# Optimization experiments

Measured on AMD Instinct MI355X. Metric: run time of the kernel, lower is better.

The kernel has to match this reference:

```python
import jax, jax.numpy as jnp
import numpy as np

T, B, L = 40, 64, 80
D_IN = 256
H = 4 * D_IN  # 1024
A = 18


def _lstm_scan(x, h0, c0, W_ih, W_hh, b_ih, b_hh):
    # x: [S,B,in] -> outputs [S,B,H]; PyTorch gate order i,f,g,o
    b = b_ih + b_hh
    def step(carry, xt):
        h, c = carry
        g = xt @ W_ih.T + h @ W_hh.T + b
        i, f, gg, o = jnp.split(g, 4, axis=-1)
        c = jax.nn.sigmoid(f) * c + jax.nn.sigmoid(i) * jnp.tanh(gg)
        h = jax.nn.sigmoid(o) * jnp.tanh(c)
        return (h, c), h
    (h, c), ys = jax.lax.scan(step, (h0, c0), x)
    return ys, h, c


def setup_inputs() -> dict:
    key = jax.random.key(0)
    ks = jax.random.split(key, 24)
    def rn(k, shape, scale=0.02):
        return jax.random.normal(k, shape, dtype=jnp.float32) * scale
    return {
        "state": rn(ks[0], (T, B, D_IN), 1.0),
        "demonstration": rn(ks[1], (T, B, L, D_IN), 1.0),
        "demonstration_length": jax.random.randint(ks[2], (T, B), 1, L + 1, dtype=jnp.int32),
        "h0": jnp.zeros((B, H), jnp.float32),
        "c0": jnp.zeros((B, H), jnp.float32),
        "enc_Wih": rn(ks[3], (4 * H, D_IN)),
        "enc_Whh": rn(ks[4], (4 * H, H)),
        "enc_bih": rn(ks[5], (4 * H,)),
        "enc_bhh": rn(ks[6], (4 * H,)),
        "attn_W": rn(ks[7], (1, 2 * H)),
        "attn_b": rn(ks[8], (1,)),
        "comb_W": rn(ks[9], (H, H + D_IN)),
        "comb_b": rn(ks[10], (H,)),
        "lstm_Wih": rn(ks[11], (4 * H, H)),
        "lstm_Whh": rn(ks[12], (4 * H, H)),
        "lstm_bih": rn(ks[13], (4 * H,)),
        "lstm_bhh": rn(ks[14], (4 * H,)),
        "mid_W": rn(ks[15], (H, H)),
        "mid_b": rn(ks[16], (H,)),
        "out_W": rn(ks[17], (A, H)),
        "out_b": rn(ks[18], (A,)),
    }


def reference(state, demonstration, demonstration_length, h0, c0,
              enc_Wih, enc_Whh, enc_bih, enc_bhh,
              attn_W, attn_b, comb_W, comb_b,
              lstm_Wih, lstm_Whh, lstm_bih, lstm_bhh,
              mid_W, mid_b, out_W, out_b):
    lengths = demonstration_length[0]              # [B], only t=0 lengths used (as in original)
    demo0 = demonstration[0]                       # [B,L,D_IN], only t=0 demo used
    z = jnp.zeros((B, H), demo0.dtype)
    enc, _, _ = _lstm_scan(demo0.transpose(1, 0, 2), z, z,
                           enc_Wih, enc_Whh, enc_bih, enc_bhh)  # [L,B,H]
    enc = enc.transpose(1, 0, 2)                   # [B,L,H]
    mask = jnp.arange(L)[None, :] < lengths[:, None]  # [B,L]
    # attn(cat(enc, h)) == enc @ Wd^T + h @ Wh^T + b (split of the concat linear)
    Wd, Wh = attn_W[:, :H], attn_W[:, H:]          # [1,H] each
    score_d = (enc @ Wd.T)[..., 0] + attn_b[0]     # [B,L], constant over t
    lstm_b = lstm_bih + lstm_bhh

    def step(carry, obs_t):
        h, c = carry
        scores = score_d + h @ Wh.T                # [B,L] ([B,1] broadcast)
        scores = jnp.where(mask, scores, -jnp.inf)
        w = jax.nn.softmax(scores, axis=-1)        # masked softmax over demo steps
        attn_applied = jnp.einsum('bl,blh->bh', w, enc)
        x = jax.nn.relu(jnp.concatenate([attn_applied, obs_t], axis=-1) @ comb_W.T + comb_b)
        g = x @ lstm_Wih.T + h @ lstm_Whh.T + lstm_b
        i, f, gg, o = jnp.split(g, 4, axis=-1)
        c = jax.nn.sigmoid(f) * c + jax.nn.sigmoid(i) * jnp.tanh(gg)
        h = jax.nn.sigmoid(o) * jnp.tanh(c)
        m = h @ mid_W.T + mid_b                    # no activation between middle and output (as in source)
        q_t = m @ out_W.T + out_b
        return (h, c), q_t

    (h, c), q = jax.lax.scan(step, (h0, c0), state)  # q: [T,B,A]
    return q, h, c
```

## Files before the change

### kernel.cpp

```cpp
#include <hip/hip_runtime.h>
#include <hip/hip_bf16.h>

#define TT 40
#define BB 64
#define LL 80
#define DD 256
#define HH 1024
#define G4H 4096
#define AA 18
#define KENC 1280
#define KLSTM 2048
#define KCOMB 1280
#define QSZ (TT*BB*AA)

typedef __bf16 bf16x8 __attribute__((ext_vector_type(8)));
typedef float  f32x4  __attribute__((ext_vector_type(4)));

#define OFF_WENC   ((size_t)0)
#define OFF_WLSTM  (OFF_WENC  + (size_t)G4H*KENC*2)
#define OFF_WCOMB  (OFF_WLSTM + (size_t)G4H*KLSTM*2)
#define OFF_WMID   (OFF_WCOMB + (size_t)HH*KCOMB*2)
#define OFF_BIASE  (OFF_WMID  + (size_t)HH*HH*2)
#define OFF_BIASL  (OFF_BIASE + (size_t)G4H*4)
#define OFF_DEMO   (OFF_BIASL + (size_t)G4H*4)
#define OFF_STATE  (OFF_DEMO  + (size_t)BB*LL*DD*2)
#define OFF_ENC    (OFF_STATE + (size_t)TT*BB*DD*2)
#define OFF_HDEC   (OFF_ENC   + (size_t)BB*LL*HH*2)
#define OFF_XALL   (OFF_HDEC  + (size_t)TT*BB*HH*2)
#define OFF_MF     (OFF_XALL  + (size_t)TT*BB*HH*2)
#define OFF_ATTNS  (OFF_MF    + (size_t)TT*BB*HH*2)
#define OFF_CF     (OFF_ATTNS + (size_t)BB*HH*2)
#define OFF_HBUF   (OFF_CF    + (size_t)BB*HH*4)

__device__ __forceinline__ float sigm(float x){ return 1.f/(1.f+__expf(-x)); }

__device__ __forceinline__ float wred_sum(float v){
#pragma unroll
  for (int s=32; s>0; s>>=1) v += __shfl_xor(v, s, 64);
  return v;
}
__device__ __forceinline__ float wred_max(float v){
#pragma unroll
  for (int s=32; s>0; s>>=1) v = fmaxf(v, __shfl_xor(v, s, 64));
  return v;
}
__device__ __forceinline__ unsigned pack_bf16(float a, float b){
  unsigned short ua = __builtin_bit_cast(unsigned short, (__bf16)a);
  unsigned short ub = __builtin_bit_cast(unsigned short, (__bf16)b);
  return (unsigned)ua | ((unsigned)ub << 16);
}

#define PB1 4096
#define PB2 8192
#define PB3 13312
#define PB4 17408
#define PB5 22528
#define PB6 25088
#define PB7 25344
#define PGRID 25472
__global__ __launch_bounds__(256)
void k_prep(const float* __restrict__ enc_wih, const float* __restrict__ enc_whh,
            const float* __restrict__ enc_bih, const float* __restrict__ enc_bhh,
            const float* __restrict__ lstm_wih, const float* __restrict__ lstm_whh,
            const float* __restrict__ lstm_bih, const float* __restrict__ lstm_bhh,
            const float* __restrict__ comb_w, const float* __restrict__ mid_w,
            const float* __restrict__ demo, const float* __restrict__ state,
            char* __restrict__ ws){
  int blk = blockIdx.x, tid = threadIdx.x;
  if (blk < PB1) {
    int p = blk;
    int gate = p & 3, jj = (p >> 2) & 3, bq = p >> 4;
    int orig = gate*HH + bq*4 + jj;
    if (tid == 0) ((float*)(ws + OFF_BIASE))[p] = enc_bih[orig] + enc_bhh[orig];
    const float* s0 = enc_wih + (size_t)orig*DD;
    const float* s1 = enc_whh + (size_t)orig*HH;
    __bf16* d = (__bf16*)(ws + OFF_WENC) + (size_t)p*KENC;
    for (int k = tid; k < KENC; k += 256)
      d[k] = (__bf16)(k < DD ? s0[k] : s1[k-DD]);
  } else if (blk < PB2) {
    int p = blk - PB1;
    int gate = p & 3, jj = (p >> 2) & 3, bq = p >> 4;
    int orig = gate*HH + bq*4 + jj;
    if (tid == 0) ((float*)(ws + OFF_BIASL))[p] = lstm_bih[orig] + lstm_bhh[orig];
    const float* s0 = lstm_wih + (size_t)orig*HH;
    const float* s1 = lstm_whh + (size_t)orig*HH;
    __bf16* d = (__bf16*)(ws + OFF_WLSTM) + (size_t)p*KLSTM;
    for (int k = tid; k < KLSTM; k += 256)
      d[k] = (__bf16)(k < HH ? s0[k] : s1[k-HH]);
  } else if (blk < PB3) {
    int i = (blk - PB2)*256 + tid;
    ((__bf16*)(ws + OFF_WCOMB))[i] = (__bf16)comb_w[i];
  } else if (blk < PB4) {
    int i = (blk - PB3)*256 + tid;
    ((__bf16*)(ws + OFF_WMID))[i] = (__bf16)mid_w[i];
  } else if (blk < PB5) {
    int i = (blk - PB4)*256 + tid;
    ((__bf16*)(ws + OFF_DEMO))[i] = (__bf16)demo[i];
  } else if (blk < PB6) {
    int i = (blk - PB5)*256 + tid;
    ((__bf16*)(ws + OFF_STATE))[i] = (__bf16)state[i];
  } else if (blk < PB7) {
    int i = (blk - PB6)*256 + tid;
    ((float*)(ws + OFF_CF))[i] = 0.f;
  } else {
    int i = (blk - PB7)*256 + tid;
    ((unsigned*)(ws + OFF_HBUF))[i] = 0u;
  }
}

__global__ __launch_bounds__(1024)
void k_enc_step(const __bf16* __restrict__ demoC, const __bf16* __restrict__ wEnc,
                const float* __restrict__ bE, const __bf16* __restrict__ hR,
                __bf16* __restrict__ hW, __bf16* __restrict__ encB,
                float* __restrict__ cf, int t){
  const int bk = blockIdx.x, tid = threadIdx.x;
  const int wv = tid >> 6, ln = tid & 63;
  const int l15 = ln & 15, lhi = ln >> 4;
  const int klane = lhi * 8;
  const int mt = wv & 3, kq = wv >> 2;
  const int am = mt*16 + l15;

  __shared__ float g_lds[4][BB*17];

  const __bf16* brow = wEnc + (size_t)(bk*16 + l15)*KENC;
  const __bf16* arow = demoC + ((size_t)am*LL + t)*DD;
  const __bf16* hrow = hR + (size_t)am*HH;

  f32x4 acc = {0.f,0.f,0.f,0.f};
  const int kb = kq*320;
#pragma unroll
  for (int kk = 0; kk < 320; kk += 32) {
    int k0 = kb + kk + klane;
    const __bf16* pa = (k0 < DD) ? (arow + k0) : (hrow + (k0 - DD));
    acc = __builtin_amdgcn_mfma_f32_16x16x32_bf16(*(const bf16x8*)pa,
                                                  *(const bf16x8*)(brow + k0), acc, 0,0,0);
  }
  {
    int r0 = mt*16 + lhi*4;
#pragma unroll
    for (int r = 0; r < 4; ++r) g_lds[kq][(r0+r)*17 + l15] = acc[r];
  }
  __syncthreads();
  if (tid < 128) {
    const int m_ = tid >> 1, q2 = tid & 1;
    const int j0_ = bk*4 + 2*q2;
    int gb = m_*17 + q2*8, cb = bk*16 + q2*8;
    float g[8];
#pragma unroll
    for (int j = 0; j < 8; ++j)
      g[j] = g_lds[0][gb+j] + g_lds[1][gb+j] + g_lds[2][gb+j] + g_lds[3][gb+j] + bE[cb+j];
    float cA = cf[m_*HH + j0_], cB = cf[m_*HH + j0_ + 1];
    float cn0 = sigm(g[1])*cA + sigm(g[0])*tanhf(g[2]);
    float cn1 = sigm(g[5])*cB + sigm(g[4])*tanhf(g[6]);
    float hn0 = sigm(g[3])*tanhf(cn0);
    float hn1 = sigm(g[7])*tanhf(cn1);
    cf[m_*HH + j0_] = cn0; cf[m_*HH + j0_ + 1] = cn1;
    unsigned hp = pack_bf16(hn0, hn1);
    *(unsigned*)(hW + (size_t)m_*HH + j0_) = hp;
    *(unsigned*)(encB + ((size_t)m_*LL + t)*HH + j0_) = hp;
  }
}

__global__ __launch_bounds__(1024)
void k_dec_step(const __bf16* __restrict__ xall, const __bf16* __restrict__ wLstm,
                const float* __restrict__ bL, const __bf16* __restrict__ hR,
                __bf16* __restrict__ hW, __bf16* __restrict__ hdec,
                float* __restrict__ cf, float* __restrict__ out, int t){
  const int bk = blockIdx.x, tid = threadIdx.x;
  const int wv = tid >> 6, ln = tid & 63;
  const int l15 = ln & 15, lhi = ln >> 4;
  const int klane = lhi * 8;
  const int mt = wv & 3, kq = wv >> 2;
  const int am = mt*16 + l15;

  __shared__ float g_lds[4][BB*17];

  const __bf16* brow = wLstm + (size_t)(bk*16 + l15)*KLSTM + kq*512;
  const __bf16* arow = (kq < 2) ? (xall + ((size_t)t*BB + am)*HH + kq*512)
                                : (hR + (size_t)am*HH + (kq-2)*512);

  f32x4 acc = {0.f,0.f,0.f,0.f};
#pragma unroll
  for (int kk = 0; kk < 512; kk += 32) {
    int k0 = kk + klane;
    acc = __builtin_amdgcn_mfma_f32_16x16x32_bf16(*(const bf16x8*)(arow + k0),
                                                  *(const bf16x8*)(brow + k0), acc, 0,0,0);
  }
  {
    int r0 = mt*16 + lhi*4;
#pragma unroll
    for (int r = 0; r < 4; ++r) g_lds[kq][(r0+r)*17 + l15] = acc[r];
  }
  __syncthreads();
  if (tid < 128) {
    const int m_ = tid >> 1, q2 = tid & 1;
    const int j0_ = bk*4 + 2*q2;
    int gb = m_*17 + q2*8, cb = bk*16 + q2*8;
    float g[8];
#pragma unroll
    for (int j = 0; j < 8; ++j)
      g[j] = g_lds[0][gb+j] + g_lds[1][gb+j] + g_lds[2][gb+j] + g_lds[3][gb+j] + bL[cb+j];
    float cA = cf[m_*HH + j0_], cB = cf[m_*HH + j0_ + 1];
    float cn0 = sigm(g[1])*cA + sigm(g[0])*tanhf(g[2]);
    float cn1 = sigm(g[5])*cB + sigm(g[4])*tanhf(g[6]);
    float hn0 = sigm(g[3])*tanhf(cn0);
    float hn1 = sigm(g[7])*tanhf(cn1);
    cf[m_*HH + j0_] = cn0; cf[m_*HH + j0_ + 1] = cn1;
    unsigned hp = pack_bf16(hn0, hn1);
    *(unsigned*)(hW + (size_t)m_*HH + j0_) = hp;
    *(unsigned*)(hdec + ((size_t)t*BB + m_)*HH + j0_) = hp;
    if (t == TT-1) {
      out[QSZ + m_*HH + j0_]     = hn0;
      out[QSZ + m_*HH + j0_ + 1] = hn1;
    }
  }
}

__global__ __launch_bounds__(256)
void k_attn(const int* __restrict__ demlen, const float* __restrict__ h0,
            const float* __restrict__ c0, const float* __restrict__ attn_w,
            const __bf16* __restrict__ encB, __bf16* __restrict__ attnS,
            __bf16* __restrict__ hD0, float* __restrict__ cf){
  const int bk = blockIdx.x, tid = threadIdx.x;
  const int wv = tid >> 6, ln = tid & 63;
  __shared__ float sc_sh[LL];
  __shared__ float w_sh[LL];
  int b = bk >> 2, qq = bk & 3;
  for (int i = 0; i < 20; ++i) {
    int l = wv*20 + i;
    const __bf16* er = encB + ((size_t)b*LL + l)*HH + ln*16;
    bf16x8 e0 = *(const bf16x8*)(er);
    bf16x8 e1 = *(const bf16x8*)(er + 8);
    float part = 0.f;
#pragma unroll
    for (int j = 0; j < 8; ++j) {
      part += (float)e0[j] * attn_w[ln*16 + j];
      part += (float)e1[j] * attn_w[ln*16 + 8 + j];
    }
    part = wred_sum(part);
    if (ln == 0) sc_sh[l] = part;
  }
  __syncthreads();
  if (wv == 0) {
    int len = demlen[b];
    float s0 = (ln < len) ? sc_sh[ln] : -1e30f;
    float s1 = (ln < 16 && 64+ln < len) ? sc_sh[64+ln] : -1e30f;
    float mx = wred_max(fmaxf(s0, s1));
    float e0 = __expf(s0 - mx);
    float e1 = (ln < 16) ? __expf(s1 - mx) : 0.f;
    float inv = 1.f / wred_sum(e0 + e1);
    w_sh[ln] = e0 * inv;
    if (ln < 16) w_sh[64+ln] = e1 * inv;
  }
  __syncthreads();
  {
    int col = qq*256 + tid;
    float a = 0.f;
    const __bf16* eb = encB + (size_t)b*LL*HH + col;
#pragma unroll 4
    for (int l = 0; l < LL; ++l) a += w_sh[l] * (float)eb[(size_t)l*HH];
    attnS[(size_t)b*HH + col] = (__bf16)a;
  }
  int gtid = bk*256 + tid;
  for (int i = gtid; i < BB*HH/2; i += 256*256) {
    int i2 = i*2;
    *((unsigned*)hD0 + i) = pack_bf16(h0[i2], h0[i2+1]);
  }
  for (int i = gtid; i < BB*HH; i += 256*256) cf[i] = c0[i];
}

__global__ __launch_bounds__(256)
void k_x(const __bf16* __restrict__ attnS, const __bf16* __restrict__ stateB,
         const __bf16* __restrict__ wComb, const float* __restrict__ comb_b,
         __bf16* __restrict__ xall){
  const int bk = blockIdx.x, tid = threadIdx.x;
  const int wv = tid >> 6, ln = tid & 63;
  const int l15 = ln & 15, lhi = ln >> 4;
  const int klane = lhi * 8;
  int g = bk*4 + wv;
  for (int i = 0; i < 10; ++i) {
    int ti = i*1024 + g;
    int mtt = ti >> 6, nt = ti & 63;
    f32x4 acc = {0.f,0.f,0.f,0.f};
    const __bf16* brow = wComb + (size_t)(nt*16 + l15)*KCOMB;
    int r = mtt*16 + l15, bb = r & 63;
    const __bf16* aat = attnS + (size_t)bb*HH;
    const __bf16* ast = stateB + (size_t)r*DD;
#pragma unroll 8
    for (int kk = 0; kk < KCOMB; kk += 32) {
      int k0 = kk + klane;
      bf16x8 af = (k0 < HH) ? *(const bf16x8*)(aat + k0)
                            : *(const bf16x8*)(ast + (k0-HH));
      acc = __builtin_amdgcn_mfma_f32_16x16x32_bf16(af, *(const bf16x8*)(brow + k0), acc, 0,0,0);
    }
    int col = nt*16 + l15;
    float cb = comb_b[col];
    int r0 = mtt*16 + lhi*4;
#pragma unroll
    for (int rr = 0; rr < 4; ++rr)
      xall[(size_t)(r0+rr)*HH + col] = (__bf16)fmaxf(acc[rr]+cb, 0.f);
  }
}

__global__ __launch_bounds__(256)
void k_mid(const __bf16* __restrict__ hdec, const __bf16* __restrict__ wMid,
           const float* __restrict__ mid_b, __bf16* __restrict__ mf){
  const int bk = blockIdx.x, tid = threadIdx.x;
  const int wv = tid >> 6, ln = tid & 63;
  const int l15 = ln & 15, lhi = ln >> 4;
  const int klane = lhi * 8;
  int g = bk*4 + wv;
  for (int i = 0; i < 10; ++i) {
    int ti = i*1024 + g;
    int mtt = ti >> 6, nt = ti & 63;
    f32x4 acc = {0.f,0.f,0.f,0.f};
    const __bf16* brow = wMid + (size_t)(nt*16 + l15)*HH;
    const __bf16* arow = hdec + (size_t)(mtt*16 + l15)*HH;
#pragma unroll 8
    for (int kk = 0; kk < HH; kk += 32) {
      int k0 = kk + klane;
      acc = __builtin_amdgcn_mfma_f32_16x16x32_bf16(*(const bf16x8*)(arow + k0),
                                                    *(const bf16x8*)(brow + k0), acc, 0,0,0);
    }
    int col = nt*16 + l15;
    float mb = mid_b[col];
    int r0 = mtt*16 + lhi*4;
#pragma unroll
    for (int rr = 0; rr < 4; ++rr)
      mf[(size_t)(r0+rr)*HH + col] = (__bf16)(acc[rr]+mb);
  }
}

__global__ __launch_bounds__(256)
void k_out(const __bf16* __restrict__ mf, const float* __restrict__ out_w,
           const float* __restrict__ out_b, const float* __restrict__ cf,
           float* __restrict__ out){
  const int bk = blockIdx.x, tid = threadIdx.x;
  const int wv = tid >> 6, ln = tid & 63;
  int g = bk*4 + wv;
  for (int i = 0; i < 3; ++i) {
    int row = i*1024 + g;
    if (row < TT*BB) {
      const __bf16* mr = mf + (size_t)row*HH;
      float mreg[16];
#pragma unroll
      for (int k = 0; k < 16; ++k) mreg[k] = (float)mr[ln + 64*k];
      for (int a = 0; a < AA; ++a) {
        float p = 0.f;
#pragma unroll
        for (int k = 0; k < 16; ++k) p += mreg[k] * out_w[(size_t)a*HH + ln + 64*k];
        p = wred_sum(p);
        if (ln == 0) out[(size_t)row*AA + a] = p + out_b[a];
      }
    }
  }
  for (int i = bk*256 + tid; i < BB*HH; i += 256*256)
    out[QSZ + BB*HH + i] = cf[i];
}

extern "C" void kernel_launch(void* const* d_in, const int* in_sizes, int n_in,
                              void* d_out, int out_size, void* d_ws, size_t ws_size,
                              hipStream_t stream) {
  (void)in_sizes; (void)n_in; (void)out_size; (void)ws_size;
  const float* state    = (const float*)d_in[0];
  const float* demo     = (const float*)d_in[1];
  const int*   demlen   = (const int*)d_in[2];
  const float* h0       = (const float*)d_in[3];
  const float* c0       = (const float*)d_in[4];
  const float* enc_wih  = (const float*)d_in[5];
  const float* enc_whh  = (const float*)d_in[6];
  const float* enc_bih  = (const float*)d_in[7];
  const float* enc_bhh  = (const float*)d_in[8];
  const float* attn_w   = (const float*)d_in[9];
  const float* comb_w   = (const float*)d_in[11];
  const float* comb_b   = (const float*)d_in[12];
  const float* lstm_wih = (const float*)d_in[13];
  const float* lstm_whh = (const float*)d_in[14];
  const float* lstm_bih = (const float*)d_in[15];
  const float* lstm_bhh = (const float*)d_in[16];
  const float* mid_w    = (const float*)d_in[17];
  const float* mid_b    = (const float*)d_in[18];
  const float* out_w    = (const float*)d_in[19];
  const float* out_b    = (const float*)d_in[20];
  char* ws = (char*)d_ws;

  __bf16* wEnc  = (__bf16*)(ws + OFF_WENC);
  __bf16* wLstm = (__bf16*)(ws + OFF_WLSTM);
  __bf16* wComb = (__bf16*)(ws + OFF_WCOMB);
  __bf16* wMid  = (__bf16*)(ws + OFF_WMID);
  float*  bE    = (float*)(ws + OFF_BIASE);
  float*  bL    = (float*)(ws + OFF_BIASL);
  __bf16* demoC = (__bf16*)(ws + OFF_DEMO);
  __bf16* stateB= (__bf16*)(ws + OFF_STATE);
  __bf16* encB  = (__bf16*)(ws + OFF_ENC);
  __bf16* hdec  = (__bf16*)(ws + OFF_HDEC);
  __bf16* xall  = (__bf16*)(ws + OFF_XALL);
  __bf16* mf    = (__bf16*)(ws + OFF_MF);
  __bf16* attnS = (__bf16*)(ws + OFF_ATTNS);
  float*  cf    = (float*)(ws + OFF_CF);
  __bf16* hbE0  = (__bf16*)(ws + OFF_HBUF);
  __bf16* hbE1  = hbE0 + (size_t)BB*HH;
  __bf16* hbD0  = hbE1 + (size_t)BB*HH;
  __bf16* hbD1  = hbD0 + (size_t)BB*HH;
  float*  out   = (float*)d_out;

  k_prep<<<PGRID, 256, 0, stream>>>(enc_wih, enc_whh, enc_bih, enc_bhh,
                                    lstm_wih, lstm_whh, lstm_bih, lstm_bhh,
                                    comb_w, mid_w, demo, state, ws);
  for (int t = 0; t < LL; ++t) {
    __bf16* hR = (t & 1) ? hbE1 : hbE0;
    __bf16* hW = (t & 1) ? hbE0 : hbE1;
    k_enc_step<<<256, 1024, 0, stream>>>(demoC, wEnc, bE, hR, hW, encB, cf, t);
  }
  k_attn<<<256, 256, 0, stream>>>(demlen, h0, c0, attn_w, encB, attnS, hbD0, cf);
  k_x<<<256, 256, 0, stream>>>(attnS, stateB, wComb, comb_b, xall);
  for (int t = 0; t < TT; ++t) {
    __bf16* hR = (t & 1) ? hbD1 : hbD0;
    __bf16* hW = (t & 1) ? hbD0 : hbD1;
    k_dec_step<<<256, 1024, 0, stream>>>(xall, wLstm, bL, hR, hW, hdec, cf, out, t);
  }
  k_mid<<<256, 256, 0, stream>>>(hdec, wMid, mid_b, mf);
  k_out<<<256, 256, 0, stream>>>(mf, out_w, out_b, cf, out);
}
```

Before: 1.910 ms.

## Replace per-step LSTM launches with persistent kernels using per-group flag barriers

The 80 encoder and 40 decoder per-timestep launches become two persistent kernels of 512 blocks. The batch is split into 8 independent groups of 8 rows, and each group syncs through flag-based barriers, so only blocks sharing batch rows wait on each other. The cell state now lives in registers, and h is written to a rotating per-timestep buffer with system-coherent stores. This removes launch overhead and global c round-trips, but wastes half of each 16-row MFMA tile, relies on all 512 blocks being co-resident, and has a spin timeout that could silently break correctness.

```diff
diff --git a/kernel.cpp b/kernel.cpp
--- a/kernel.cpp
+++ b/kernel.cpp
@@ -12,6 +12,13 @@
 #define KLSTM 2048
 #define KCOMB 1280
 #define QSZ (TT*BB*AA)
+
+#define GROUPS 8
+#define GBLK 64
+#define NBLK (GROUPS*GBLK)
+#define NSLOT_E (LL+1)
+#define NSLOT_D (TT+1)
+#define FLAG_STRIDE 16
 
 typedef __bf16 bf16x8 __attribute__((ext_vector_type(8)));
 typedef float  f32x4  __attribute__((ext_vector_type(4)));
@@ -29,8 +36,8 @@
 #define OFF_XALL   (OFF_HDEC  + (size_t)TT*BB*HH*2)
 #define OFF_MF     (OFF_XALL  + (size_t)TT*BB*HH*2)
 #define OFF_ATTNS  (OFF_MF    + (size_t)TT*BB*HH*2)
-#define OFF_CF     (OFF_ATTNS + (size_t)BB*HH*2)
-#define OFF_HBUF   (OFF_CF    + (size_t)BB*HH*4)
+#define OFF_HROT   (OFF_ATTNS + (size_t)BB*HH*2)
+#define OFF_BAR    (OFF_HROT  + (size_t)GROUPS*(NSLOT_E+NSLOT_D)*8*HH*2)
 
 __device__ __forceinline__ float sigm(float x){ return 1.f/(1.f+__expf(-x)); }
 
@@ -44,10 +51,34 @@
   for (int s=32; s>0; s>>=1) v = fmaxf(v, __shfl_xor(v, s, 64));
   return v;
 }
-__device__ __forceinline__ unsigned pack_bf16(float a, float b){
-  unsigned short ua = __builtin_bit_cast(unsigned short, (__bf16)a);
-  unsigned short ub = __builtin_bit_cast(unsigned short, (__bf16)b);
-  return (unsigned)ua | ((unsigned)ub << 16);
+
+__device__ __forceinline__ void st_b16_sc(__bf16* p, float v){
+  unsigned short u = __builtin_bit_cast(unsigned short, (__bf16)v);
+  asm volatile("global_store_short %0, %1, off sc0 sc1"
+               :: "v"(p), "v"((unsigned)u) : "memory");
+}
+
+__device__ __forceinline__ void grp_arrive(unsigned* flags, unsigned target, int bk){
+  __syncthreads();
+  if (threadIdx.x == 0) {
+    __builtin_amdgcn_fence(__ATOMIC_RELEASE, "agent");
+    __hip_atomic_store(flags + (size_t)bk*FLAG_STRIDE, target,
+                       __ATOMIC_RELAXED, __HIP_MEMORY_SCOPE_AGENT);
+  }
+}
+__device__ __forceinline__ void grp_wait(unsigned* flags, unsigned target, int g){
+  if (threadIdx.x < 64) {
+    unsigned long long spins = 0;
+    for (;;) {
+      unsigned a = __hip_atomic_load(flags + (size_t)(g*GBLK + threadIdx.x)*FLAG_STRIDE,
+                                     __ATOMIC_RELAXED, __HIP_MEMORY_SCOPE_AGENT);
+      if (__all((int)(a >= target))) break;
+      if (++spins > (1ull<<20)) break;
+      __builtin_amdgcn_s_sleep(1);
+    }
+  }
+  __syncthreads();
+  asm volatile("" ::: "memory");
 }
 
 #define PB1 4096
@@ -56,8 +87,8 @@
 #define PB4 17408
 #define PB5 22528
 #define PB6 25088
-#define PB7 25344
-#define PGRID 25472
+#define PB7 25216
+#define PGRID 25280
 __global__ __launch_bounds__(256)
 void k_prep(const float* __restrict__ enc_wih, const float* __restrict__ enc_whh,
             const float* __restrict__ enc_bih, const float* __restrict__ enc_bhh,
@@ -101,126 +132,138 @@
     ((__bf16*)(ws + OFF_STATE))[i] = (__bf16)state[i];
   } else if (blk < PB7) {
     int i = (blk - PB6)*256 + tid;
-    ((float*)(ws + OFF_CF))[i] = 0.f;
+    int g = i >> 12, r = i & 4095;
+    ((unsigned*)(ws + OFF_HROT))[(size_t)g*(NSLOT_E*8*HH/2) + r] = 0u;
   } else {
     int i = (blk - PB7)*256 + tid;
-    ((unsigned*)(ws + OFF_HBUF))[i] = 0u;
-  }
-}
-
-__global__ __launch_bounds__(1024)
-void k_enc_step(const __bf16* __restrict__ demoC, const __bf16* __restrict__ wEnc,
-                const float* __restrict__ bE, const __bf16* __restrict__ hR,
-                __bf16* __restrict__ hW, __bf16* __restrict__ encB,
-                float* __restrict__ cf, int t){
-  const int bk = blockIdx.x, tid = threadIdx.x;
+    ((unsigned*)(ws + OFF_BAR))[i] = 0u;
+  }
+}
+
+__global__ __launch_bounds__(256, 2)
+void k_enc(const __bf16* __restrict__ demoC, const __bf16* __restrict__ wEnc,
+           const float* __restrict__ bE, __bf16* __restrict__ hrotE,
+           __bf16* __restrict__ encB, unsigned* __restrict__ flagsE){
+  const int bk = blockIdx.x, tid = threadIdx.x;
+  const int g = bk >> 6, b64 = bk & 63;
   const int wv = tid >> 6, ln = tid & 63;
   const int l15 = ln & 15, lhi = ln >> 4;
   const int klane = lhi * 8;
-  const int mt = wv & 3, kq = wv >> 2;
-  const int am = mt*16 + l15;
-
-  __shared__ float g_lds[4][BB*17];
-
-  const __bf16* brow = wEnc + (size_t)(bk*16 + l15)*KENC;
-  const __bf16* arow = demoC + ((size_t)am*LL + t)*DD;
-  const __bf16* hrow = hR + (size_t)am*HH;
-
-  f32x4 acc = {0.f,0.f,0.f,0.f};
-  const int kb = kq*320;
-#pragma unroll
-  for (int kk = 0; kk < 320; kk += 32) {
-    int k0 = kb + kk + klane;
-    const __bf16* pa = (k0 < DD) ? (arow + k0) : (hrow + (k0 - DD));
-    acc = __builtin_amdgcn_mfma_f32_16x16x32_bf16(*(const bf16x8*)pa,
-                                                  *(const bf16x8*)(brow + k0), acc, 0,0,0);
-  }
-  {
-    int r0 = mt*16 + lhi*4;
-#pragma unroll
-    for (int r = 0; r < 4; ++r) g_lds[kq][(r0+r)*17 + l15] = acc[r];
-  }
-  __syncthreads();
-  if (tid < 128) {
-    const int m_ = tid >> 1, q2 = tid & 1;
-    const int j0_ = bk*4 + 2*q2;
-    int gb = m_*17 + q2*8, cb = bk*16 + q2*8;
-    float g[8];
-#pragma unroll
-    for (int j = 0; j < 8; ++j)
-      g[j] = g_lds[0][gb+j] + g_lds[1][gb+j] + g_lds[2][gb+j] + g_lds[3][gb+j] + bE[cb+j];
-    float cA = cf[m_*HH + j0_], cB = cf[m_*HH + j0_ + 1];
-    float cn0 = sigm(g[1])*cA + sigm(g[0])*tanhf(g[2]);
-    float cn1 = sigm(g[5])*cB + sigm(g[4])*tanhf(g[6]);
-    float hn0 = sigm(g[3])*tanhf(cn0);
-    float hn1 = sigm(g[7])*tanhf(cn1);
-    cf[m_*HH + j0_] = cn0; cf[m_*HH + j0_ + 1] = cn1;
-    unsigned hp = pack_bf16(hn0, hn1);
-    *(unsigned*)(hW + (size_t)m_*HH + j0_) = hp;
-    *(unsigned*)(encB + ((size_t)m_*LL + t)*HH + j0_) = hp;
-  }
-}
-
-__global__ __launch_bounds__(1024)
-void k_dec_step(const __bf16* __restrict__ xall, const __bf16* __restrict__ wLstm,
-                const float* __restrict__ bL, const __bf16* __restrict__ hR,
-                __bf16* __restrict__ hW, __bf16* __restrict__ hdec,
-                float* __restrict__ cf, float* __restrict__ out, int t){
-  const int bk = blockIdx.x, tid = threadIdx.x;
+  const int mb = l15 & 7;
+  const int batch = g*8 + mb;
+
+  __shared__ float g_lds[8][68];
+
+  const __bf16* brow = wEnc + (size_t)(b64*64 + wv*16 + l15)*KENC;
+  const __bf16* drow = demoC + (size_t)batch*LL*DD;
+  __bf16* hbase = hrotE + (size_t)g*NSLOT_E*8*HH;
+
+  const int em = tid >> 4, ec = tid & 15;
+  const int ecol = b64*16 + ec;
+  const int ebatch = g*8 + em;
+  float creg = 0.f;
+
+  for (int t = 0; t < LL; ++t) {
+    const __bf16* hR = hbase + (size_t)t*8*HH + (size_t)mb*HH;
+    const __bf16* arow = drow + (size_t)t*DD;
+    f32x4 acc = {0.f,0.f,0.f,0.f};
+#pragma unroll 8
+    for (int kk = 0; kk < KENC; kk += 32) {
+      int k0 = kk + klane;
+      const __bf16* pa = (k0 < DD) ? (arow + k0) : (hR + (k0 - DD));
+      acc = __builtin_amdgcn_mfma_f32_16x16x32_bf16(*(const bf16x8*)pa,
+                                                    *(const bf16x8*)(brow + k0), acc, 0,0,0);
+    }
+    {
+      int r0 = lhi*4;
+#pragma unroll
+      for (int r = 0; r < 4; ++r) {
+        int row = r0 + r;
+        if (row < 8) g_lds[row][wv*16 + l15] = acc[r];
+      }
+    }
+    __syncthreads();
+    if (tid < 128) {
+      int pb = b64*64 + ec*4;
+      float gi = g_lds[em][ec*4+0] + bE[pb+0];
+      float gf = g_lds[em][ec*4+1] + bE[pb+1];
+      float gg = g_lds[em][ec*4+2] + bE[pb+2];
+      float go = g_lds[em][ec*4+3] + bE[pb+3];
+      creg = sigm(gf)*creg + sigm(gi)*tanhf(gg);
+      float hn = sigm(go)*tanhf(creg);
+      st_b16_sc(hbase + (size_t)(t+1)*8*HH + (size_t)em*HH + ecol, hn);
+      encB[((size_t)ebatch*LL + t)*HH + ecol] = (__bf16)hn;
+    }
+    grp_arrive(flagsE, (unsigned)(t+1), bk);
+    grp_wait(flagsE, (unsigned)(t+1), g);
+  }
+}
+
+__global__ __launch_bounds__(256, 2)
+void k_dec(const __bf16* __restrict__ xall, const __bf16* __restrict__ wLstm,
+           const float* __restrict__ bL, const float* __restrict__ c0,
+           __bf16* __restrict__ hrotD, __bf16* __restrict__ hdec,
+           float* __restrict__ out, unsigned* __restrict__ flagsD){
+  const int bk = blockIdx.x, tid = threadIdx.x;
+  const int g = bk >> 6, b64 = bk & 63;
   const int wv = tid >> 6, ln = tid & 63;
   const int l15 = ln & 15, lhi = ln >> 4;
   const int klane = lhi * 8;
-  const int mt = wv & 3, kq = wv >> 2;
-  const int am = mt*16 + l15;
-
-  __shared__ float g_lds[4][BB*17];
-
-  const __bf16* brow = wLstm + (size_t)(bk*16 + l15)*KLSTM + kq*512;
-  const __bf16* arow = (kq < 2) ? (xall + ((size_t)t*BB + am)*HH + kq*512)
-                                : (hR + (size_t)am*HH + (kq-2)*512);
-
-  f32x4 acc = {0.f,0.f,0.f,0.f};
-#pragma unroll
-  for (int kk = 0; kk < 512; kk += 32) {
-    int k0 = kk + klane;
-    acc = __builtin_amdgcn_mfma_f32_16x16x32_bf16(*(const bf16x8*)(arow + k0),
-                                                  *(const bf16x8*)(brow + k0), acc, 0,0,0);
-  }
-  {
-    int r0 = mt*16 + lhi*4;
-#pragma unroll
-    for (int r = 0; r < 4; ++r) g_lds[kq][(r0+r)*17 + l15] = acc[r];
-  }
-  __syncthreads();
-  if (tid < 128) {
-    const int m_ = tid >> 1, q2 = tid & 1;
-    const int j0_ = bk*4 + 2*q2;
-    int gb = m_*17 + q2*8, cb = bk*16 + q2*8;
-    float g[8];
-#pragma unroll
-    for (int j = 0; j < 8; ++j)
-      g[j] = g_lds[0][gb+j] + g_lds[1][gb+j] + g_lds[2][gb+j] + g_lds[3][gb+j] + bL[cb+j];
-    float cA = cf[m_*HH + j0_], cB = cf[m_*HH + j0_ + 1];
-    float cn0 = sigm(g[1])*cA + sigm(g[0])*tanhf(g[2]);
-    float cn1 = sigm(g[5])*cB + sigm(g[4])*tanhf(g[6]);
-    float hn0 = sigm(g[3])*tanhf(cn0);
-    float hn1 = sigm(g[7])*tanhf(cn1);
-    cf[m_*HH + j0_] = cn0; cf[m_*HH + j0_ + 1] = cn1;
-    unsigned hp = pack_bf16(hn0, hn1);
-    *(unsigned*)(hW + (size_t)m_*HH + j0_) = hp;
-    *(unsigned*)(hdec + ((size_t)t*BB + m_)*HH + j0_) = hp;
-    if (t == TT-1) {
-      out[QSZ + m_*HH + j0_]     = hn0;
-      out[QSZ + m_*HH + j0_ + 1] = hn1;
-    }
-  }
+  const int mb = l15 & 7;
+  const int batch = g*8 + mb;
+
+  __shared__ float g_lds[8][68];
+
+  const __bf16* brow = wLstm + (size_t)(b64*64 + wv*16 + l15)*KLSTM;
+  __bf16* hbase = hrotD + (size_t)g*NSLOT_D*8*HH;
+
+  const int em = tid >> 4, ec = tid & 15;
+  const int ecol = b64*16 + ec;
+  const int ebatch = g*8 + em;
+  float creg = (tid < 128) ? c0[(size_t)ebatch*HH + ecol] : 0.f;
+
+  for (int t = 0; t < TT; ++t) {
+    const __bf16* hR = hbase + (size_t)t*8*HH + (size_t)mb*HH;
+    const __bf16* xrow = xall + ((size_t)t*BB + batch)*HH;
+    f32x4 acc = {0.f,0.f,0.f,0.f};
+#pragma unroll 8
+    for (int kk = 0; kk < KLSTM; kk += 32) {
+      int k0 = kk + klane;
+      const __bf16* pa = (k0 < HH) ? (xrow + k0) : (hR + (k0 - HH));
+      acc = __builtin_amdgcn_mfma_f32_16x16x32_bf16(*(const bf16x8*)pa,
+                                                    *(const bf16x8*)(brow + k0), acc, 0,0,0);
+    }
+    {
+      int r0 = lhi*4;
+#pragma unroll
+      for (int r = 0; r < 4; ++r) {
+        int row = r0 + r;
+        if (row < 8) g_lds[row][wv*16 + l15] = acc[r];
+      }
+    }
+    __syncthreads();
+    if (tid < 128) {
+      int pb = b64*64 + ec*4;
+      float gi = g_lds[em][ec*4+0] + bL[pb+0];
+      float gf = g_lds[em][ec*4+1] + bL[pb+1];
+      float gg = g_lds[em][ec*4+2] + bL[pb+2];
+      float go = g_lds[em][ec*4+3] + bL[pb+3];
+      creg = sigm(gf)*creg + sigm(gi)*tanhf(gg);
+      float hn = sigm(go)*tanhf(creg);
+      st_b16_sc(hbase + (size_t)(t+1)*8*HH + (size_t)em*HH + ecol, hn);
+      hdec[((size_t)t*BB + ebatch)*HH + ecol] = (__bf16)hn;
+      if (t == TT-1) out[QSZ + (size_t)ebatch*HH + ecol] = hn;
+    }
+    grp_arrive(flagsD, (unsigned)(t+1), bk);
+    grp_wait(flagsD, (unsigned)(t+1), g);
+  }
+  if (tid < 128) out[QSZ + BB*HH + (size_t)ebatch*HH + ecol] = creg;
 }
 
 __global__ __launch_bounds__(256)
 void k_attn(const int* __restrict__ demlen, const float* __restrict__ h0,
-            const float* __restrict__ c0, const float* __restrict__ attn_w,
-            const __bf16* __restrict__ encB, __bf16* __restrict__ attnS,
-            __bf16* __restrict__ hD0, float* __restrict__ cf){
+            const float* __restrict__ attn_w, const __bf16* __restrict__ encB,
+            __bf16* __restrict__ attnS, __bf16* __restrict__ hrotD){
   const int bk = blockIdx.x, tid = threadIdx.x;
   const int wv = tid >> 6, ln = tid & 63;
   __shared__ float sc_sh[LL];
@@ -261,12 +304,11 @@
     for (int l = 0; l < LL; ++l) a += w_sh[l] * (float)eb[(size_t)l*HH];
     attnS[(size_t)b*HH + col] = (__bf16)a;
   }
-  int gtid = bk*256 + tid;
-  for (int i = gtid; i < BB*HH/2; i += 256*256) {
-    int i2 = i*2;
-    *((unsigned*)hD0 + i) = pack_bf16(h0[i2], h0[i2+1]);
-  }
-  for (int i = gtid; i < BB*HH; i += 256*256) cf[i] = c0[i];
+  for (int i = bk*256 + tid; i < BB*HH; i += 256*256) {
+    int bb2 = i >> 10, col = i & 1023;
+    int gg2 = bb2 >> 3, mm2 = bb2 & 7;
+    hrotD[((size_t)gg2*NSLOT_D*8 + mm2)*HH + col] = (__bf16)h0[i];
+  }
 }
 
 __global__ __launch_bounds__(256)
@@ -333,8 +375,7 @@
 
 __global__ __launch_bounds__(256)
 void k_out(const __bf16* __restrict__ mf, const float* __restrict__ out_w,
-           const float* __restrict__ out_b, const float* __restrict__ cf,
-           float* __restrict__ out){
+           const float* __restrict__ out_b, float* __restrict__ out){
   const int bk = blockIdx.x, tid = threadIdx.x;
   const int wv = tid >> 6, ln = tid & 63;
   int g = bk*4 + wv;
@@ -354,8 +395,6 @@
       }
     }
   }
-  for (int i = bk*256 + tid; i < BB*HH; i += 256*256)
-    out[QSZ + BB*HH + i] = cf[i];
 }
 
 extern "C" void kernel_launch(void* const* d_in, const int* in_sizes, int n_in,
@@ -397,28 +436,19 @@
   __bf16* xall  = (__bf16*)(ws + OFF_XALL);
   __bf16* mf    = (__bf16*)(ws + OFF_MF);
   __bf16* attnS = (__bf16*)(ws + OFF_ATTNS);
-  float*  cf    = (float*)(ws + OFF_CF);
-  __bf16* hbE0  = (__bf16*)(ws + OFF_HBUF);
-  __bf16* hbE1  = hbE0 + (size_t)BB*HH;
-  __bf16* hbD0  = hbE1 + (size_t)BB*HH;
-  __bf16* hbD1  = hbD0 + (size_t)BB*HH;
+  __bf16* hrotE = (__bf16*)(ws + OFF_HROT);
+  __bf16* hrotD = hrotE + (size_t)GROUPS*NSLOT_E*8*HH;
+  unsigned* flagsE = (unsigned*)(ws + OFF_BAR);
+  unsigned* flagsD = flagsE + (size_t)NBLK*FLAG_STRIDE;
   float*  out   = (float*)d_out;
 
   k_prep<<<PGRID, 256, 0, stream>>>(enc_wih, enc_whh, enc_bih, enc_bhh,
                                     lstm_wih, lstm_whh, lstm_bih, lstm_bhh,
                                     comb_w, mid_w, demo, state, ws);
-  for (int t = 0; t < LL; ++t) {
-    __bf16* hR = (t & 1) ? hbE1 : hbE0;
-    __bf16* hW = (t & 1) ? hbE0 : hbE1;
-    k_enc_step<<<256, 1024, 0, stream>>>(demoC, wEnc, bE, hR, hW, encB, cf, t);
-  }
-  k_attn<<<256, 256, 0, stream>>>(demlen, h0, c0, attn_w, encB, attnS, hbD0, cf);
+  k_enc<<<NBLK, 256, 0, stream>>>(demoC, wEnc, bE, hrotE, encB, flagsE);
+  k_attn<<<256, 256, 0, stream>>>(demlen, h0, attn_w, encB, attnS, hrotD);
   k_x<<<256, 256, 0, stream>>>(attnS, stateB, wComb, comb_b, xall);
-  for (int t = 0; t < TT; ++t) {
-    __bf16* hR = (t & 1) ? hbD1 : hbD0;
-    __bf16* hW = (t & 1) ? hbD0 : hbD1;
-    k_dec_step<<<256, 1024, 0, stream>>>(xall, wLstm, bL, hR, hW, hdec, cf, out, t);
-  }
+  k_dec<<<NBLK, 256, 0, stream>>>(xall, wLstm, bL, c0, hrotD, hdec, out, flagsD);
   k_mid<<<256, 256, 0, stream>>>(hdec, wMid, mid_b, mf);
-  k_out<<<256, 256, 0, stream>>>(mf, out_w, out_b, cf, out);
-}
+  k_out<<<256, 256, 0, stream>>>(mf, out_w, out_b, out);
+}
```

Result: slower. 3.686 ms (+93.0%).
